# Optimization experiments

Measured on AMD Instinct MI355X. Metric: run time of the kernel, lower is better.

## Reference

```python
import jax, jax.numpy as jnp
import numpy as np

B, T, H, U = 32, 2048, 1024, 1024

def setup_inputs() -> dict:
    key = jax.random.key(0)
    ks = jax.random.split(key, 8)
    s = 1.0 / np.sqrt(H)
    return {
        "dec_hidden": jax.random.normal(ks[0], (B, H), jnp.float32),
        "all_enc_hiddens": jax.random.normal(ks[1], (B, T, H), jnp.float32),
        "W1": jax.random.normal(ks[2], (H, U), jnp.float32) * s,
        "b1": jnp.zeros((U,), jnp.float32),
        "W2": jax.random.normal(ks[3], (H, U), jnp.float32) * s,
        "b2": jnp.zeros((U,), jnp.float32),
        "V": jax.random.normal(ks[4], (U, 1), jnp.float32) * (1.0 / np.sqrt(U)),
        "bv": jnp.zeros((1,), jnp.float32),
    }

def reference(dec_hidden, all_enc_hiddens, W1, b1, W2, b2, V, bv):
    # query projection: [B, 1, U]
    q = (dec_hidden @ W1 + b1)[:, None, :]
    # key projection: [B, T, U]
    k = jnp.einsum("bth,hu->btu", all_enc_hiddens, W2) + b2
    # additive score: [B, T, 1]
    score = jnp.tanh(q + k) @ V + bv
    # softmax over time axis
    attn = jax.nn.softmax(score, axis=1)  # [B, T, 1]
    # weighted context: [B, H]
    context = jnp.sum(attn * all_enc_hiddens, axis=1)
    return (context, attn)
```

## Files before the change

### kernel.cpp

```cpp
#include <hip/hip_runtime.h>
#include <hip/hip_bf16.h>
#include <math.h>

#define B_SZ 32
#define T_SZ 2048
#define H_SZ 1024
#define U_SZ 1024

#define BM 64
#define BN 256
#define BK 64
#define UT_N (U_SZ / BN)

typedef __attribute__((ext_vector_type(8))) short bf16x8;
typedef __attribute__((ext_vector_type(4))) float f32x4;

__device__ __forceinline__ unsigned int f2bf(float f) {
  union { float f; unsigned int u; } x; x.f = f;
  unsigned int r = x.u + 0x7FFFu + ((x.u >> 16) & 1u);
  return r >> 16;
}

__device__ __forceinline__ float bf2f(unsigned int lo16) {
  union { unsigned int u; float f; } x; x.u = lo16 << 16; return x.f;
}

__device__ __forceinline__ void async_cp16(const unsigned short* g, unsigned short* l) {
  __builtin_amdgcn_global_load_lds(
      (const __attribute__((address_space(1))) unsigned int*)g,
      (__attribute__((address_space(3))) unsigned int*)l, 16, 0, 0);
}

__device__ __forceinline__ float fast_tanh(float x) {
  const float e = __expf(x + x);
  return (e - 1.0f) * __builtin_amdgcn_rcpf(e + 1.0f);
}

__global__ __launch_bounds__(256) void k_prep(
    const float* __restrict__ enc, unsigned short* __restrict__ encb,
    const float* __restrict__ W2, unsigned short* __restrict__ W2t,
    const float* __restrict__ dec, const float* __restrict__ W1,
    const float* __restrict__ b1, const float* __restrict__ b2,
    float* __restrict__ qq, int cvtN)
{
  __shared__ char lds_raw[64 * 65 * 2];
  const int bid = blockIdx.x;
  const int tid = threadIdx.x;

  if (bid < cvtN) {
    const size_t i = ((size_t)bid * 256 + tid) * 8;
    const float4 a = *(const float4*)(enc + i);
    const float4 b = *(const float4*)(enc + i + 4);
    uint4 o;
    o.x = f2bf(a.x) | (f2bf(a.y) << 16);
    o.y = f2bf(a.z) | (f2bf(a.w) << 16);
    o.z = f2bf(b.x) | (f2bf(b.y) << 16);
    o.w = f2bf(b.z) | (f2bf(b.w) << 16);
    *(uint4*)(encb + i) = o;
  } else if (bid < cvtN + 256) {
    unsigned short (*tile)[65] = (unsigned short(*)[65])lds_raw;
    const int idx = bid - cvtN;
    const int bu = idx & 15, bh = idx >> 4;
    const int tc = tid & 63, tr = tid >> 6;
    #pragma unroll
    for (int i = 0; i < 16; ++i) {
      const int hl = tr + i * 4;
      tile[tc][hl] = (unsigned short)f2bf(W2[(size_t)(bh * 64 + hl) * U_SZ + bu * 64 + tc]);
    }
    __syncthreads();
    #pragma unroll
    for (int i = 0; i < 16; ++i) {
      const int ul = tr + i * 4;
      W2t[(size_t)(bu * 64 + ul) * H_SZ + bh * 64 + tc] = tile[ul][tc];
    }
  } else {
    float (*red)[64] = (float(*)[64])lds_raw;
    const int idx = bid - (cvtN + 256);
    const int ul = tid & 63;
    const int hq = tid >> 6;
    const int u  = (idx & 15) * 64 + ul;
    const int b  = idx >> 4;
    const float* dh = dec + b * H_SZ + hq * 256;
    const float* w  = W1 + (size_t)(hq * 256) * U_SZ + u;
    float acc = 0.0f;
    #pragma unroll 8
    for (int h = 0; h < 256; ++h) acc += dh[h] * w[(size_t)h * U_SZ];
    red[hq][ul] = acc;
    __syncthreads();
    if (tid < 64) {
      const float s = red[0][ul] + red[1][ul] + red[2][ul] + red[3][ul];
      qq[b * U_SZ + u] = s + b1[u] + b2[u];
    }
  }
}

template <bool PRE_BF16>
__global__ __launch_bounds__(256) void k_gemm_score(
    const unsigned short* __restrict__ encb,
    const float* __restrict__ encf,
    const unsigned short* __restrict__ W2t,
    const float* __restrict__ qq, const float* __restrict__ Vv,
    float* __restrict__ score)
{
  __shared__ unsigned short Al[BM * BK];
  __shared__ unsigned short Bl[BN * BK];
  __shared__ float scoreS[BM];

  const int tid  = threadIdx.x;
  const int wave = tid >> 6;
  const int lane = tid & 63;
  const int quad = lane >> 4;
  const int l16  = lane & 15;
  const int m0   = blockIdx.x * BM;
  const int b    = m0 >> 11;

  if (tid < BM) scoreS[tid] = 0.0f;

  size_t aoff[2]; unsigned short* dstA[2];
  #pragma unroll
  for (int i = 0; i < 2; ++i) {
    const int slot = (i * 4 + wave) * 64 + lane;
    const int r = slot >> 3;
    const int c = ((slot & 7) - r) & 7;
    aoff[i] = (size_t)(m0 + r) * H_SZ + c * 8;
    dstA[i] = &Al[(i * 4 + wave) * 512];
  }
  size_t boff[8]; unsigned short* dstB[8];
  #pragma unroll
  for (int i = 0; i < 8; ++i) {
    const int slot = (i * 4 + wave) * 64 + lane;
    const int r = slot >> 3;
    const int c = ((slot & 7) - r) & 7;
    boff[i] = (size_t)r * H_SZ + c * 8;
    dstB[i] = &Bl[(i * 4 + wave) * 512];
  }

  const int ar[4] = { 0 * 16 + l16, 1 * 16 + l16, 2 * 16 + l16, 3 * 16 + l16 };
  const int bu[4] = { wave * 64 + 0 * 16 + l16, wave * 64 + 1 * 16 + l16,
                      wave * 64 + 2 * 16 + l16, wave * 64 + 3 * 16 + l16 };

  for (int ut = 0; ut < UT_N; ++ut) {
    const int u0 = ut * BN;
    f32x4 acc[4][4];
    #pragma unroll
    for (int rt = 0; rt < 4; ++rt)
      #pragma unroll
      for (int ct = 0; ct < 4; ++ct)
        #pragma unroll
        for (int r = 0; r < 4; ++r) acc[rt][ct][r] = 0.0f;

    for (int kk = 0; kk < H_SZ; kk += BK) {
      __syncthreads();
      if constexpr (PRE_BF16) {
        #pragma unroll
        for (int i = 0; i < 2; ++i) async_cp16(encb + aoff[i] + kk, dstA[i]);
      } else {
        #pragma unroll
        for (int i = 0; i < 2; ++i) {
          const int slot = i * 256 + tid;
          const int r = slot >> 3;
          const int c = ((slot & 7) - r) & 7;
          const float* src = encf + (size_t)(m0 + r) * H_SZ + kk + c * 8;
          const float4 x = *(const float4*)src;
          const float4 y = *(const float4*)(src + 4);
          uint4 o;
          o.x = f2bf(x.x) | (f2bf(x.y) << 16);
          o.y = f2bf(x.z) | (f2bf(x.w) << 16);
          o.z = f2bf(y.x) | (f2bf(y.y) << 16);
          o.w = f2bf(y.z) | (f2bf(y.w) << 16);
          *(uint4*)&Al[slot * 8] = o;
        }
      }
      #pragma unroll
      for (int i = 0; i < 8; ++i)
        async_cp16(W2t + (size_t)u0 * H_SZ + boff[i] + kk, dstB[i]);
      __syncthreads();

      #pragma unroll
      for (int h = 0; h < 2; ++h) {
        bf16x8 af[4], bfr[4];
        #pragma unroll
        for (int rt = 0; rt < 4; ++rt)
          af[rt] = *(const bf16x8*)&Al[ar[rt] * 64 + ((h * 4 + quad + ar[rt]) & 7) * 8];
        #pragma unroll
        for (int ct = 0; ct < 4; ++ct)
          bfr[ct] = *(const bf16x8*)&Bl[bu[ct] * 64 + ((h * 4 + quad + bu[ct]) & 7) * 8];
        #pragma unroll
        for (int rt = 0; rt < 4; ++rt)
          #pragma unroll
          for (int ct = 0; ct < 4; ++ct)
            acc[rt][ct] = __builtin_amdgcn_mfma_f32_16x16x32_bf16(
                af[rt], bfr[ct], acc[rt][ct], 0, 0, 0);
      }
    }

    float part[4][4];
    #pragma unroll
    for (int rt = 0; rt < 4; ++rt)
      #pragma unroll
      for (int r = 0; r < 4; ++r) part[rt][r] = 0.0f;
    #pragma unroll
    for (int ct = 0; ct < 4; ++ct) {
      const int u = u0 + wave * 64 + ct * 16 + l16;
      const float qv = qq[b * U_SZ + u];
      const float vv = Vv[u];
      #pragma unroll
      for (int rt = 0; rt < 4; ++rt)
        #pragma unroll
        for (int r = 0; r < 4; ++r)
          part[rt][r] += fast_tanh(acc[rt][ct][r] + qv) * vv;
    }
    #pragma unroll
    for (int rt = 0; rt < 4; ++rt)
      #pragma unroll
      for (int r = 0; r < 4; ++r) {
        float p = part[rt][r];
        p += __shfl_xor(p, 1);
        p += __shfl_xor(p, 2);
        p += __shfl_xor(p, 4);
        p += __shfl_xor(p, 8);
        part[rt][r] = p;
      }
    if (l16 == 0) {
      #pragma unroll
      for (int rt = 0; rt < 4; ++rt)
        #pragma unroll
        for (int r = 0; r < 4; ++r)
          atomicAdd(&scoreS[rt * 16 + quad * 4 + r], part[rt][r]);
    }
  }
  __syncthreads();
  if (tid < BM) score[m0 + tid] = scoreS[tid];
}

__global__ void k_softmax(const float* __restrict__ score, float* __restrict__ attn) {
  const int b = blockIdx.x;
  const int tid = threadIdx.x;
  __shared__ float wmax[4], wsum[4];
  const float* s = score + b * T_SZ;
  float v[8];
  float lmax = -INFINITY;
  #pragma unroll
  for (int i = 0; i < 8; ++i) { v[i] = s[tid + i * 256]; lmax = fmaxf(lmax, v[i]); }
  #pragma unroll
  for (int m = 1; m <= 32; m <<= 1) lmax = fmaxf(lmax, __shfl_xor(lmax, m));
  if ((tid & 63) == 0) wmax[tid >> 6] = lmax;
  __syncthreads();
  const float gmax = fmaxf(fmaxf(wmax[0], wmax[1]), fmaxf(wmax[2], wmax[3]));
  float lsum = 0.0f;
  #pragma unroll
  for (int i = 0; i < 8; ++i) { v[i] = __expf(v[i] - gmax); lsum += v[i]; }
  #pragma unroll
  for (int m = 1; m <= 32; m <<= 1) lsum += __shfl_xor(lsum, m);
  if ((tid & 63) == 0) wsum[tid >> 6] = lsum;
  __syncthreads();
  const float inv = 1.0f / (wsum[0] + wsum[1] + wsum[2] + wsum[3]);
  #pragma unroll
  for (int i = 0; i < 8; ++i) attn[b * T_SZ + tid + i * 256] = v[i] * inv;
}

__global__ void k_context_bf16(const unsigned short* __restrict__ encb,
                               const float* __restrict__ attn, float* __restrict__ ctx) {
  const int tcx = blockIdx.x;
  const int hc  = blockIdx.y;
  const int b   = blockIdx.z;
  const int h0  = hc * 512 + threadIdx.x * 2;
  const unsigned short* e = encb + ((size_t)b * T_SZ + tcx * 256) * H_SZ + h0;
  const float* a = attn + b * T_SZ + tcx * 256;
  float c0 = 0, c1 = 0;
  #pragma unroll 4
  for (int t = 0; t < 256; ++t) {
    const unsigned int v = *(const unsigned int*)&e[(size_t)t * H_SZ];
    c0 += a[t] * bf2f(v & 0xFFFFu);
    c1 += a[t] * bf2f(v >> 16);
  }
  atomicAdd(&ctx[b * H_SZ + h0],     c0);
  atomicAdd(&ctx[b * H_SZ + h0 + 1], c1);
}

__global__ void k_context_f32(const float* __restrict__ enc,
                              const float* __restrict__ attn, float* __restrict__ ctx) {
  const int tcx = blockIdx.x, hc = blockIdx.y, b = blockIdx.z;
  const int h = hc * 256 + threadIdx.x;
  const float* e = enc + ((size_t)b * T_SZ + tcx * 256) * H_SZ + h;
  const float* a = attn + b * T_SZ + tcx * 256;
  float a0 = 0, a1 = 0, a2 = 0, a3 = 0;
  for (int t = 0; t < 256; t += 4) {
    a0 += a[t]     * e[(size_t)t * H_SZ];
    a1 += a[t + 1] * e[(size_t)(t + 1) * H_SZ];
    a2 += a[t + 2] * e[(size_t)(t + 2) * H_SZ];
    a3 += a[t + 3] * e[(size_t)(t + 3) * H_SZ];
  }
  atomicAdd(&ctx[b * H_SZ + h], (a0 + a1) + (a2 + a3));
}

extern "C" void kernel_launch(void* const* d_in, const int* in_sizes, int n_in,
                              void* d_out, int out_size, void* d_ws, size_t ws_size,
                              hipStream_t stream) {
  const float* dec = (const float*)d_in[0];
  const float* enc = (const float*)d_in[1];
  const float* W1  = (const float*)d_in[2];
  const float* b1  = (const float*)d_in[3];
  const float* W2  = (const float*)d_in[4];
  const float* b2  = (const float*)d_in[5];
  const float* Vv  = (const float*)d_in[6];

  const size_t encb_bytes = (size_t)B_SZ * T_SZ * H_SZ * 2;
  const size_t fast_need  = encb_bytes + (2u << 20) + (128u << 10) + (256u << 10);
  const bool fast = ws_size >= fast_need;

  char* ws = (char*)d_ws;
  unsigned short* encb = nullptr;
  unsigned short* W2t;
  float *qq, *score;
  if (fast) {
    encb  = (unsigned short*)ws;
    W2t   = (unsigned short*)(ws + encb_bytes);
    qq    = (float*)(ws + encb_bytes + (2u << 20));
    score = (float*)(ws + encb_bytes + (2u << 20) + (128u << 10));
  } else {
    W2t   = (unsigned short*)ws;
    qq    = (float*)(ws + (2u << 20));
    score = (float*)(ws + (2u << 20) + (128u << 10));
  }

  float* ctx  = (float*)d_out;
  float* attn = (float*)d_out + B_SZ * H_SZ;

  hipMemsetAsync(ctx, 0, B_SZ * H_SZ * sizeof(float), stream);
  const int cvtN = fast ? (B_SZ * T_SZ * H_SZ) / (256 * 8) : 0;
  k_prep<<<cvtN + 256 + 512, 256, 0, stream>>>(enc, encb, W2, W2t,
                                               dec, W1, b1, b2, qq, cvtN);
  if (fast)
    k_gemm_score<true><<<(B_SZ * T_SZ) / BM, 256, 0, stream>>>(encb, enc, W2t, qq, Vv, score);
  else
    k_gemm_score<false><<<(B_SZ * T_SZ) / BM, 256, 0, stream>>>(encb, enc, W2t, qq, Vv, score);
  k_softmax<<<32, 256, 0, stream>>>(score, attn);
  if (fast)
    k_context_bf16<<<dim3(8, 2, 32), 256, 0, stream>>>(encb, attn, ctx);
  else
    k_context_f32<<<dim3(8, 4, 32), 256, 0, stream>>>(enc, attn, ctx);
}
```

Measured before the change: 638.7 us.

## Rewrite bf16 score GEMM with larger tiles and double-buffered async LDS pipeline

Replaces the bf16 score GEMM with a new kernel using 256-row tiles, 512 threads in 8 waves (2x4), and double-buffered LDS fed by async global-to-LDS copies. Loads for the next K step are issued before computing the current one, with explicit vmcnt waits and barriers in place of full syncthreads. The bigger row tile lets each W2 tile loaded into LDS serve four times as many rows, cutting W2 reloads from global memory. The trade-off is higher register pressure (32 accumulators per wave) and more LDS per block, which may reduce occupancy.

```diff
diff --git a/kernel.cpp b/kernel.cpp
--- a/kernel.cpp
+++ b/kernel.cpp
@@ -11,6 +11,7 @@
 #define BN 256
 #define BK 64
 #define UT_N (U_SZ / BN)
+#define BM2 256
 
 typedef __attribute__((ext_vector_type(8))) short bf16x8;
 typedef __attribute__((ext_vector_type(4))) float f32x4;
@@ -94,16 +95,151 @@
   }
 }
 
-template <bool PRE_BF16>
-__global__ __launch_bounds__(256) void k_gemm_score(
+__global__ __launch_bounds__(512, 2) void k_gemm_score2(
     const unsigned short* __restrict__ encb,
+    const unsigned short* __restrict__ W2t,
+    const float* __restrict__ qq, const float* __restrict__ Vv,
+    float* __restrict__ score)
+{
+  __shared__ unsigned short Al[2][BM2 * BK];
+  __shared__ unsigned short Bl[2][BN * BK];
+
+  const int tid  = threadIdx.x;
+  const int wid  = tid >> 6;
+  const int lane = tid & 63;
+  const int quad = lane >> 4;
+  const int l16  = lane & 15;
+  const int wr   = wid >> 2;
+  const int wc   = wid & 3;
+  const int m0   = blockIdx.x * BM2;
+  const int b    = m0 >> 11;
+
+  unsigned int aoff[4], boff[4];
+  int swi[4];
+  #pragma unroll
+  for (int j = 0; j < 4; ++j) {
+    const int sw = j * 8 + wid;
+    const int s  = sw * 64 + lane;
+    const int r  = s >> 3;
+    const int c  = ((s & 7) - r) & 7;
+    aoff[j] = (unsigned int)((m0 + r) * H_SZ + c * 8);
+    boff[j] = (unsigned int)(r * H_SZ + c * 8);
+    swi[j]  = sw * 512;
+  }
+
+  f32x4 acc[8][4];
+  float part[8][4];
+  #pragma unroll
+  for (int rt = 0; rt < 8; ++rt)
+    #pragma unroll
+    for (int ct = 0; ct < 4; ++ct) {
+      part[rt][ct] = 0.0f;
+      #pragma unroll
+      for (int r = 0; r < 4; ++r) acc[rt][ct][r] = 0.0f;
+    }
+
+  auto STAGE = [&](int i) {
+    const int ut = i >> 4;
+    const unsigned int kk = (unsigned int)(i & 15) * 64u;
+    const int bs = i & 1;
+    #pragma unroll
+    for (int j = 0; j < 4; ++j)
+      async_cp16(encb + aoff[j] + kk, &Al[bs][swi[j]]);
+    const unsigned int uoff = (unsigned int)(ut * 256) * H_SZ + kk;
+    #pragma unroll
+    for (int j = 0; j < 4; ++j)
+      async_cp16(W2t + uoff + boff[j], &Bl[bs][swi[j]]);
+  };
+
+  auto COMPUTE = [&](int i) {
+    const unsigned short* Ab = Al[i & 1];
+    const unsigned short* Bb = Bl[i & 1];
+    #pragma unroll
+    for (int h = 0; h < 2; ++h) {
+      bf16x8 af[8], bfr[4];
+      #pragma unroll
+      for (int rt = 0; rt < 8; ++rt) {
+        const int ar = wr * 128 + rt * 16 + l16;
+        af[rt] = *(const bf16x8*)&Ab[ar * 64 + ((h * 4 + quad + ar) & 7) * 8];
+      }
+      #pragma unroll
+      for (int ct = 0; ct < 4; ++ct) {
+        const int bu = wc * 64 + ct * 16 + l16;
+        bfr[ct] = *(const bf16x8*)&Bb[bu * 64 + ((h * 4 + quad + bu) & 7) * 8];
+      }
+      #pragma unroll
+      for (int rt = 0; rt < 8; ++rt)
+        #pragma unroll
+        for (int ct = 0; ct < 4; ++ct)
+          acc[rt][ct] = __builtin_amdgcn_mfma_f32_16x16x32_bf16(
+              af[rt], bfr[ct], acc[rt][ct], 0, 0, 0);
+    }
+  };
+
+  auto EPILOGUE = [&](int ut) {
+    #pragma unroll
+    for (int ct = 0; ct < 4; ++ct) {
+      const int u = ut * 256 + wc * 64 + ct * 16 + l16;
+      const float qv = qq[b * U_SZ + u];
+      const float vv = Vv[u];
+      #pragma unroll
+      for (int rt = 0; rt < 8; ++rt)
+        #pragma unroll
+        for (int r = 0; r < 4; ++r)
+          part[rt][r] += fast_tanh(acc[rt][ct][r] + qv) * vv;
+    }
+    #pragma unroll
+    for (int rt = 0; rt < 8; ++rt)
+      #pragma unroll
+      for (int ct = 0; ct < 4; ++ct)
+        #pragma unroll
+        for (int r = 0; r < 4; ++r) acc[rt][ct][r] = 0.0f;
+  };
+
+  STAGE(0);
+  for (int i = 0; i < 63; ++i) {
+    STAGE(i + 1);
+    asm volatile("s_waitcnt vmcnt(8)" ::: "memory");
+    __builtin_amdgcn_s_barrier();
+    __builtin_amdgcn_sched_barrier(0);
+    COMPUTE(i);
+    if ((i & 15) == 15) EPILOGUE(i >> 4);
+    __builtin_amdgcn_sched_barrier(0);
+    __builtin_amdgcn_s_barrier();
+  }
+  asm volatile("s_waitcnt vmcnt(0)" ::: "memory");
+  __builtin_amdgcn_s_barrier();
+  __builtin_amdgcn_sched_barrier(0);
+  COMPUTE(63);
+  EPILOGUE(3);
+
+  __syncthreads();
+  float* scoreS = (float*)&Al[0][0];
+  if (tid < BM2) scoreS[tid] = 0.0f;
+  __syncthreads();
+  #pragma unroll
+  for (int rt = 0; rt < 8; ++rt)
+    #pragma unroll
+    for (int r = 0; r < 4; ++r) {
+      float p = part[rt][r];
+      p += __shfl_xor(p, 1);
+      p += __shfl_xor(p, 2);
+      p += __shfl_xor(p, 4);
+      p += __shfl_xor(p, 8);
+      if (l16 == 0) atomicAdd(&scoreS[wr * 128 + rt * 16 + quad * 4 + r], p);
+    }
+  __syncthreads();
+  if (tid < BM2) score[m0 + tid] = scoreS[tid];
+}
+
+__global__ __launch_bounds__(256) void k_gemm_score_f32(
     const float* __restrict__ encf,
     const unsigned short* __restrict__ W2t,
     const float* __restrict__ qq, const float* __restrict__ Vv,
     float* __restrict__ score)
 {
-  __shared__ unsigned short Al[BM * BK];
-  __shared__ unsigned short Bl[BN * BK];
+  __shared__ unsigned short Alo[BM * BK];
+  __shared__ unsigned short Blo[BN * BK];
   __shared__ float scoreS[BM];
 
   const int tid  = threadIdx.x;
@@ -116,15 +252,6 @@
 
   if (tid < BM) scoreS[tid] = 0.0f;
 
-  size_t aoff[2]; unsigned short* dstA[2];
-  #pragma unroll
-  for (int i = 0; i < 2; ++i) {
-    const int slot = (i * 4 + wave) * 64 + lane;
-    const int r = slot >> 3;
-    const int c = ((slot & 7) - r) & 7;
-    aoff[i] = (size_t)(m0 + r) * H_SZ + c * 8;
-    dstA[i] = &Al[(i * 4 + wave) * 512];
-  }
   size_t boff[8]; unsigned short* dstB[8];
   #pragma unroll
   for (int i = 0; i < 8; ++i) {
@@ -132,7 +259,7 @@
     const int r = slot >> 3;
     const int c = ((slot & 7) - r) & 7;
     boff[i] = (size_t)r * H_SZ + c * 8;
-    dstB[i] = &Bl[(i * 4 + wave) * 512];
+    dstB[i] = &Blo[(i * 4 + wave) * 512];
   }
 
   const int ar[4] = { 0 * 16 + l16, 1 * 16 + l16, 2 * 16 + l16, 3 * 16 + l16 };
@@ -151,25 +278,20 @@
 
     for (int kk = 0; kk < H_SZ; kk += BK) {
       __syncthreads();
-      if constexpr (PRE_BF16) {
-        #pragma unroll
-        for (int i = 0; i < 2; ++i) async_cp16(encb + aoff[i] + kk, dstA[i]);
-      } else {
-        #pragma unroll
-        for (int i = 0; i < 2; ++i) {
-          const int slot = i * 256 + tid;
-          const int r = slot >> 3;
-          const int c = ((slot & 7) - r) & 7;
-          const float* src = encf + (size_t)(m0 + r) * H_SZ + kk + c * 8;
-          const float4 x = *(const float4*)src;
-          const float4 y = *(const float4*)(src + 4);
-          uint4 o;
-          o.x = f2bf(x.x) | (f2bf(x.y) << 16);
-          o.y = f2bf(x.z) | (f2bf(x.w) << 16);
-          o.z = f2bf(y.x) | (f2bf(y.y) << 16);
-          o.w = f2bf(y.z) | (f2bf(y.w) << 16);
-          *(uint4*)&Al[slot * 8] = o;
-        }
+      #pragma unroll
+      for (int i = 0; i < 2; ++i) {
+        const int slot = i * 256 + tid;
+        const int r = slot >> 3;
+        const int c = ((slot & 7) - r) & 7;
+        const float* src = encf + (size_t)(m0 + r) * H_SZ + kk + c * 8;
+        const float4 x = *(const float4*)src;
+        const float4 y = *(const float4*)(src + 4);
+        uint4 o;
+        o.x = f2bf(x.x) | (f2bf(x.y) << 16);
+        o.y = f2bf(x.z) | (f2bf(x.w) << 16);
+        o.z = f2bf(y.x) | (f2bf(y.y) << 16);
+        o.w = f2bf(y.z) | (f2bf(y.w) << 16);
+        *(uint4*)&Alo[slot * 8] = o;
       }
       #pragma unroll
       for (int i = 0; i < 8; ++i)
@@ -181,10 +303,10 @@
         bf16x8 af[4], bfr[4];
         #pragma unroll
         for (int rt = 0; rt < 4; ++rt)
-          af[rt] = *(const bf16x8*)&Al[ar[rt] * 64 + ((h * 4 + quad + ar[rt]) & 7) * 8];
+          af[rt] = *(const bf16x8*)&Alo[ar[rt] * 64 + ((h * 4 + quad + ar[rt]) & 7) * 8];
         #pragma unroll
         for (int ct = 0; ct < 4; ++ct)
-          bfr[ct] = *(const bf16x8*)&Bl[bu[ct] * 64 + ((h * 4 + quad + bu[ct]) & 7) * 8];
+          bfr[ct] = *(const bf16x8*)&Blo[bu[ct] * 64 + ((h * 4 + quad + bu[ct]) & 7) * 8];
         #pragma unroll
         for (int rt = 0; rt < 4; ++rt)
           #pragma unroll
@@ -332,9 +454,9 @@
   k_prep<<<cvtN + 256 + 512, 256, 0, stream>>>(enc, encb, W2, W2t,
                                                dec, W1, b1, b2, qq, cvtN);
   if (fast)
-    k_gemm_score<true><<<(B_SZ * T_SZ) / BM, 256, 0, stream>>>(encb, enc, W2t, qq, Vv, score);
+    k_gemm_score2<<<(B_SZ * T_SZ) / BM2, 512, 0, stream>>>(encb, W2t, qq, Vv, score);
   else
-    k_gemm_score<false><<<(B_SZ * T_SZ) / BM, 256, 0, stream>>>(encb, enc, W2t, qq, Vv, score);
+    k_gemm_score_f32<<<(B_SZ * T_SZ) / BM, 256, 0, stream>>>(enc, W2t, qq, Vv, score);
   k_softmax<<<32, 256, 0, stream>>>(score, attn);
   if (fast)
     k_context_bf16<<<dim3(8, 2, 32), 256, 0, stream>>>(encb, attn, ctx);
```

Measured after the change: 599.4 us. 1.07x faster.
